# Performance work log

Hardware: AMD Instinct MI355X
Metric: run time of the kernel (lower is better)

Reference implementation:

```python
import jax, jax.numpy as jnp
import numpy as np

N, IN_F, OUT_F = 12288, 256, 128

def setup_inputs() -> dict:
    key = jax.random.key(0)
    k1, k2, k3, k4 = jax.random.split(key, 4)
    x = jax.random.uniform(k1, (N, IN_F), dtype=jnp.float32)
    adj = jax.random.uniform(k2, (N, N), dtype=jnp.float32)
    W = jax.random.normal(k3, (IN_F, OUT_F), dtype=jnp.float32) * (1.0 / np.sqrt(OUT_F))
    b = jax.random.normal(k4, (OUT_F,), dtype=jnp.float32) * (1.0 / np.sqrt(OUT_F))
    return {"x": x, "adj": adj, "W": W, "b": b}

def reference(x, adj, W, b):
    # adj_hat = adj + I  (add self-loops)
    n = adj.shape[0]
    adj_hat = adj + jnp.eye(n, dtype=adj.dtype)
    # Symmetric degree normalization: D^{-1/2} adj_hat D^{-1/2}.
    # Original builds diag matrices and does two NxN matmuls; the math is
    # equivalent to a row/col broadcast scaling, which we use here.
    deg = jnp.sum(adj_hat, axis=1)                  # [N]
    d_inv_sqrt = deg ** -0.5                        # [N]
    adj_norm = adj_hat * d_inv_sqrt[:, None] * d_inv_sqrt[None, :]
    support = x @ W                                 # [N, OUT_F]
    out = adj_norm @ support + b                    # [N, OUT_F]
    return out
```

## Files before the change

### kernel.cpp

```cpp
#include <hip/hip_runtime.h>
#include <cstdint>
#include <cstddef>

#define N_NODES 12288
#define IN_F 256
#define OUT_F 128
#define BM 48
#define BK 256
#define NSTEPS (N_NODES / BK)
#define A_BYTES (BM * BK)
#define B_BYTES (OUT_F * BK)
#define SLOT (A_BYTES + B_BYTES)

using f32x4 = __attribute__((ext_vector_type(4))) float;
typedef long long i64;

__global__ __launch_bounds__(256) void k_deg(const float* __restrict__ adj,
                                             float* __restrict__ dinv,
                                             unsigned int* __restrict__ adjq) {
  const size_t row = blockIdx.x;
  const float4* p = reinterpret_cast<const float4*>(adj + row * N_NODES) + threadIdx.x;
  unsigned int* q = adjq + row * (N_NODES / 4) + threadIdx.x;
  float s = 0.f;
#pragma unroll
  for (int i = 0; i < (N_NODES / 4) / 256; ++i) {
    float4 v = p[(size_t)i * 256];
    s += (v.x + v.y) + (v.z + v.w);
    unsigned int u = (unsigned)__builtin_amdgcn_cvt_pk_fp8_f32(v.x, v.y, 0, false);
    u = (unsigned)__builtin_amdgcn_cvt_pk_fp8_f32(v.z, v.w, (int)u, true);
    q[(size_t)i * 256] = u;
  }
#pragma unroll
  for (int off = 32; off >= 1; off >>= 1) s += __shfl_down(s, off, 64);
  __shared__ float red[4];
  const int lane = threadIdx.x & 63, w = threadIdx.x >> 6;
  if (lane == 0) red[w] = s;
  __syncthreads();
  if (threadIdx.x == 0) {
    float tot = (red[0] + red[1]) + (red[2] + red[3]) + 1.0f;
    dinv[row] = rsqrtf(tot);
  }
}

__global__ __launch_bounds__(256) void k_support(const float* __restrict__ x,
                                                 const float* __restrict__ W,
                                                 const float* __restrict__ dinv,
                                                 float* __restrict__ ssc,
                                                 unsigned char* __restrict__ sTq) {
  const int r = threadIdx.x >> 5;
  const int c4 = (threadIdx.x & 31) << 2;
  const size_t row = (size_t)blockIdx.x * 8 + r;
  const float* xr = x + row * IN_F;
  float a0 = 0.f, a1 = 0.f, a2 = 0.f, a3 = 0.f;
#pragma unroll 4
  for (int k = 0; k < IN_F; ++k) {
    float xv = xr[k];
    float4 wv = *reinterpret_cast<const float4*>(W + (size_t)k * OUT_F + c4);
    a0 = fmaf(xv, wv.x, a0); a1 = fmaf(xv, wv.y, a1);
    a2 = fmaf(xv, wv.z, a2); a3 = fmaf(xv, wv.w, a3);
  }
  const float d = dinv[row];
  a0 *= d; a1 *= d; a2 *= d; a3 *= d;
  *reinterpret_cast<float4*>(ssc + row * OUT_F + c4) = make_float4(a0, a1, a2, a3);
  unsigned int u01 = (unsigned)__builtin_amdgcn_cvt_pk_fp8_f32(a0 * 64.f, a1 * 64.f, 0, false);
  unsigned int u23 = (unsigned)__builtin_amdgcn_cvt_pk_fp8_f32(a2 * 64.f, a3 * 64.f, 0, false);
  sTq[(size_t)(c4 + 0) * N_NODES + row] = (unsigned char)(u01 & 0xff);
  sTq[(size_t)(c4 + 1) * N_NODES + row] = (unsigned char)((u01 >> 8) & 0xff);
  sTq[(size_t)(c4 + 2) * N_NODES + row] = (unsigned char)(u23 & 0xff);
  sTq[(size_t)(c4 + 3) * N_NODES + row] = (unsigned char)((u23 >> 8) & 0xff);
}

__global__ __launch_bounds__(256, 1) void k_gemm(const unsigned char* __restrict__ adjq,
                                                 const unsigned char* __restrict__ sTq,
                                                 const float* __restrict__ ssc,
                                                 const float* __restrict__ dinv,
                                                 const float* __restrict__ bias,
                                                 float* __restrict__ out) {
  __shared__ __align__(16) char LDSBUF[2 * SLOT];

  const int tid = threadIdx.x;
  const int lane = tid & 63;
  const int wv = tid >> 6;
  const size_t rowbase = (size_t)blockIdx.x * BM;

  const int g = lane >> 4;
  const int c15 = lane & 15;
  const int dr = c15 & 7;

  f32x4 acc[3][2];
#pragma unroll
  for (int mt = 0; mt < 3; ++mt)
#pragma unroll
    for (int nt = 0; nt < 2; ++nt) acc[mt][nt] = (f32x4){0.f, 0.f, 0.f, 0.f};

  auto stage = [&](int s, int slot) {
    char* L = LDSBUF + slot * SLOT;
#pragma unroll
    for (int j = 0; j < 3; ++j) {
      const int instr = wv * 3 + j;
      const int r = instr * 4 + g;
      const int chunk = c15 ^ (r & 7);
      const unsigned char* src = adjq + (rowbase + r) * (size_t)N_NODES +
                                 (size_t)s * BK + chunk * 16;
      __builtin_amdgcn_global_load_lds(
          (__attribute__((address_space(1))) void*)src,
          (__attribute__((address_space(3))) void*)(L + instr * 1024 + lane * 16),
          16, 0, 0);
    }
#pragma unroll
    for (int j = 0; j < 8; ++j) {
      const int instr = wv * 8 + j;
      const int o = instr * 4 + g;
      const int chunk = c15 ^ (o & 7);
      const unsigned char* src = sTq + (size_t)o * N_NODES + (size_t)s * BK + chunk * 16;
      __builtin_amdgcn_global_load_lds(
          (__attribute__((address_space(1))) void*)src,
          (__attribute__((address_space(3))) void*)(L + A_BYTES + instr * 1024 + lane * 16),
          16, 0, 0);
    }
  };

  auto compute = [&](int slot) {
    const char* LA = LDSBUF + slot * SLOT;
    const char* LB = LA + A_BYTES;
    const int bcol0 = wv * 32 + c15;
#pragma unroll
    for (int kt = 0; kt < 8; ++kt) {
      const int phys = (((kt * 2 + (g >> 1)) ^ dr) << 4) + ((g & 1) << 3);
      i64 a0 = *(const i64*)(LA + (0 * 16 + c15) * 256 + phys);
      i64 a1 = *(const i64*)(LA + (1 * 16 + c15) * 256 + phys);
      i64 a2 = *(const i64*)(LA + (2 * 16 + c15) * 256 + phys);
      i64 b0 = *(const i64*)(LB + (size_t)(bcol0)*256 + phys);
      i64 b1 = *(const i64*)(LB + (size_t)(bcol0 + 16) * 256 + phys);
      acc[0][0] = __builtin_amdgcn_mfma_f32_16x16x32_fp8_fp8(a0, b0, acc[0][0], 0, 0, 0);
      acc[0][1] = __builtin_amdgcn_mfma_f32_16x16x32_fp8_fp8(a0, b1, acc[0][1], 0, 0, 0);
      acc[1][0] = __builtin_amdgcn_mfma_f32_16x16x32_fp8_fp8(a1, b0, acc[1][0], 0, 0, 0);
      acc[1][1] = __builtin_amdgcn_mfma_f32_16x16x32_fp8_fp8(a1, b1, acc[1][1], 0, 0, 0);
      acc[2][0] = __builtin_amdgcn_mfma_f32_16x16x32_fp8_fp8(a2, b0, acc[2][0], 0, 0, 0);
      acc[2][1] = __builtin_amdgcn_mfma_f32_16x16x32_fp8_fp8(a2, b1, acc[2][1], 0, 0, 0);
    }
  };

#define GSTEP(s, VMC, DOSTAGE)                                   \
  {                                                              \
    asm volatile("s_waitcnt vmcnt(" VMC ")" ::: "memory");       \
    __builtin_amdgcn_s_barrier();                                \
    __builtin_amdgcn_sched_barrier(0);                           \
    compute((s) & 1);                                            \
    __builtin_amdgcn_s_barrier();                                \
    __builtin_amdgcn_sched_barrier(0);                           \
    if (DOSTAGE) stage((s) + 2, (s) & 1);                        \
    __builtin_amdgcn_sched_barrier(0);                           \
  }

  stage(0, 0);
  __builtin_amdgcn_sched_barrier(0);
  stage(1, 1);

  for (int s = 0; s < NSTEPS - 2; ++s) GSTEP(s, "11", 1);
  GSTEP(NSTEPS - 2, "11", 0);
  GSTEP(NSTEPS - 1, "0", 0);
#undef GSTEP

  const float inv64 = 0.015625f;
  const int col0 = wv * 32 + c15;
#pragma unroll
  for (int mt = 0; mt < 3; ++mt) {
#pragma unroll
    for (int nt = 0; nt < 2; ++nt) {
      const int col = col0 + nt * 16;
      const float bv = bias[col];
#pragma unroll
      for (int r = 0; r < 4; ++r) {
        const size_t orow = rowbase + mt * 16 + (g << 2) + r;
        const float d = dinv[orow];
        out[orow * OUT_F + col] =
            fmaf(d, acc[mt][nt][r] * inv64 + ssc[orow * OUT_F + col], bv);
      }
    }
  }
}

extern "C" void kernel_launch(void* const* d_in, const int* in_sizes, int n_in,
                              void* d_out, int out_size, void* d_ws, size_t ws_size,
                              hipStream_t stream) {
  const float* x   = (const float*)d_in[0];
  const float* adj = (const float*)d_in[1];
  const float* W   = (const float*)d_in[2];
  const float* b   = (const float*)d_in[3];
  float* out = (float*)d_out;

  char* ws = (char*)d_ws;
  float* dinv         = (float*)ws;
  float* ssc          = (float*)(ws + 49152);
  unsigned char* sTq  = (unsigned char*)(ws + 49152 + 6291456);
  unsigned char* adjq = (unsigned char*)(ws + 49152 + 6291456 + 1572864);

  k_deg<<<N_NODES, 256, 0, stream>>>(adj, dinv, (unsigned int*)adjq);
  k_support<<<N_NODES / 8, 256, 0, stream>>>(x, W, dinv, ssc, sTq);
  k_gemm<<<256, 256, 0, stream>>>(adjq, sTq, ssc, dinv, b, out);
}
```

Before: 268.3 us.

## Shrink GEMM row tile, load B directly to registers, triple-buffer A with staggered K start

The adjacency GEMM tile drops from 48 to 16 rows, so 768 blocks launch instead of 256, with launch bounds allowing three blocks per CU. The support operand B is now loaded from global memory straight into registers, two steps ahead, instead of through LDS. Only A goes through a three-slot LDS ring. Each block starts its K loop at a different phase, spreading the B reads across cache lines. The degree kernel now uses nontemporal loads for the large fp32 adjacency read. The trade-off is more parallelism and fewer LDS trips against three times as many B reads per output row, plus much higher register pressure from the B buffers.

```diff
diff --git a/kernel.cpp b/kernel.cpp
--- a/kernel.cpp
+++ b/kernel.cpp
@@ -5,12 +5,9 @@
 #define N_NODES 12288
 #define IN_F 256
 #define OUT_F 128
-#define BM 48
+#define BM 16
 #define BK 256
 #define NSTEPS (N_NODES / BK)
-#define A_BYTES (BM * BK)
-#define B_BYTES (OUT_F * BK)
-#define SLOT (A_BYTES + B_BYTES)
 
 using f32x4 = __attribute__((ext_vector_type(4))) float;
 typedef long long i64;
@@ -19,15 +16,15 @@
                                              float* __restrict__ dinv,
                                              unsigned int* __restrict__ adjq) {
   const size_t row = blockIdx.x;
-  const float4* p = reinterpret_cast<const float4*>(adj + row * N_NODES) + threadIdx.x;
+  const f32x4* p = reinterpret_cast<const f32x4*>(adj + row * N_NODES) + threadIdx.x;
   unsigned int* q = adjq + row * (N_NODES / 4) + threadIdx.x;
   float s = 0.f;
 #pragma unroll
   for (int i = 0; i < (N_NODES / 4) / 256; ++i) {
-    float4 v = p[(size_t)i * 256];
-    s += (v.x + v.y) + (v.z + v.w);
-    unsigned int u = (unsigned)__builtin_amdgcn_cvt_pk_fp8_f32(v.x, v.y, 0, false);
-    u = (unsigned)__builtin_amdgcn_cvt_pk_fp8_f32(v.z, v.w, (int)u, true);
+    f32x4 v = __builtin_nontemporal_load(p + (size_t)i * 256);
+    s += (v[0] + v[1]) + (v[2] + v[3]);
+    unsigned int u = (unsigned)__builtin_amdgcn_cvt_pk_fp8_f32(v[0], v[1], 0, false);
+    u = (unsigned)__builtin_amdgcn_cvt_pk_fp8_f32(v[2], v[3], (int)u, true);
     q[(size_t)i * 256] = u;
   }
 #pragma unroll
@@ -70,113 +67,109 @@
   sTq[(size_t)(c4 + 3) * N_NODES + row] = (unsigned char)((u23 >> 8) & 0xff);
 }
 
-__global__ __launch_bounds__(256, 1) void k_gemm(const unsigned char* __restrict__ adjq,
+__global__ __launch_bounds__(256, 3) void k_gemm(const unsigned char* __restrict__ adjq,
                                                  const unsigned char* __restrict__ sTq,
                                                  const float* __restrict__ ssc,
                                                  const float* __restrict__ dinv,
                                                  const float* __restrict__ bias,
                                                  float* __restrict__ out) {
-  __shared__ __align__(16) char LDSBUF[2 * SLOT];
+  __shared__ __align__(16) char A_lds[3 * 4096];
 
   const int tid = threadIdx.x;
   const int lane = tid & 63;
   const int wv = tid >> 6;
   const size_t rowbase = (size_t)blockIdx.x * BM;
+  const int ph = blockIdx.x % NSTEPS;
 
   const int g = lane >> 4;
   const int c15 = lane & 15;
-  const int dr = c15 & 7;
 
-  f32x4 acc[3][2];
+  const int srow = wv * 4 + (lane >> 4);
+  const int schunk = (c15 ^ (srow & 7)) << 4;
+  const unsigned char* abase = adjq + (rowbase + srow) * (size_t)N_NODES + schunk;
+
+  const unsigned char* bptr = sTq + (size_t)(wv * 32 + c15) * N_NODES + g * 8;
+
+  f32x4 acc[2];
+  acc[0] = (f32x4){0.f, 0.f, 0.f, 0.f};
+  acc[1] = (f32x4){0.f, 0.f, 0.f, 0.f};
+
+  i64 b0[2][8], b1[2][8], b2[2][8];
+
+  auto phys = [&](int t) { int c = t + ph; if (c >= NSTEPS) c -= NSTEPS; return c; };
+
+  auto stageA = [&](int t, int slot) {
+    const int sc = phys(t);
+    __builtin_amdgcn_global_load_lds(
+        (__attribute__((address_space(1))) void*)(abase + (size_t)sc * BK),
+        (__attribute__((address_space(3))) void*)(A_lds + slot * 4096 + srow * 256 +
+                                                  (c15 << 4)),
+        16, 0, 0);
+  };
+  auto loadB = [&](int t, i64 (&B)[2][8]) {
+    const int sc = phys(t);
 #pragma unroll
-  for (int mt = 0; mt < 3; ++mt)
+    for (int nt = 0; nt < 2; ++nt)
 #pragma unroll
-    for (int nt = 0; nt < 2; ++nt) acc[mt][nt] = (f32x4){0.f, 0.f, 0.f, 0.f};
-
-  auto stage = [&](int s, int slot) {
-    char* L = LDSBUF + slot * SLOT;
+      for (int kt = 0; kt < 8; ++kt)
+        B[nt][kt] = *(const i64*)(bptr + (size_t)nt * 16 * N_NODES +
+                                  (size_t)sc * BK + kt * 32);
+  };
+  auto compute = [&](int slot, i64 (&B)[2][8]) {
+    const char* Ab = A_lds + slot * 4096 + c15 * 256;
+    const int key = c15 & 7;
 #pragma unroll
-    for (int j = 0; j < 3; ++j) {
-      const int instr = wv * 3 + j;
-      const int r = instr * 4 + g;
-      const int chunk = c15 ^ (r & 7);
-      const unsigned char* src = adjq + (rowbase + r) * (size_t)N_NODES +
-                                 (size_t)s * BK + chunk * 16;
-      __builtin_amdgcn_global_load_lds(
-          (__attribute__((address_space(1))) void*)src,
-          (__attribute__((address_space(3))) void*)(L + instr * 1024 + lane * 16),
-          16, 0, 0);
-    }
-#pragma unroll
-    for (int j = 0; j < 8; ++j) {
-      const int instr = wv * 8 + j;
-      const int o = instr * 4 + g;
-      const int chunk = c15 ^ (o & 7);
-      const unsigned char* src = sTq + (size_t)o * N_NODES + (size_t)s * BK + chunk * 16;
-      __builtin_amdgcn_global_load_lds(
-          (__attribute__((address_space(1))) void*)src,
-          (__attribute__((address_space(3))) void*)(L + A_BYTES + instr * 1024 + lane * 16),
-          16, 0, 0);
+    for (int kt = 0; kt < 8; ++kt) {
+      i64 a = *(const i64*)(Ab + (((kt * 2 + (g >> 1)) ^ key) << 4) + ((g & 1) << 3));
+      acc[0] = __builtin_amdgcn_mfma_f32_16x16x32_fp8_fp8(a, B[0][kt], acc[0], 0, 0, 0);
+      acc[1] = __builtin_amdgcn_mfma_f32_16x16x32_fp8_fp8(a, B[1][kt], acc[1], 0, 0, 0);
     }
   };
 
-  auto compute = [&](int slot) {
-    const char* LA = LDSBUF + slot * SLOT;
-    const char* LB = LA + A_BYTES;
-    const int bcol0 = wv * 32 + c15;
-#pragma unroll
-    for (int kt = 0; kt < 8; ++kt) {
-      const int phys = (((kt * 2 + (g >> 1)) ^ dr) << 4) + ((g & 1) << 3);
-      i64 a0 = *(const i64*)(LA + (0 * 16 + c15) * 256 + phys);
-      i64 a1 = *(const i64*)(LA + (1 * 16 + c15) * 256 + phys);
-      i64 a2 = *(const i64*)(LA + (2 * 16 + c15) * 256 + phys);
-      i64 b0 = *(const i64*)(LB + (size_t)(bcol0)*256 + phys);
-      i64 b1 = *(const i64*)(LB + (size_t)(bcol0 + 16) * 256 + phys);
-      acc[0][0] = __builtin_amdgcn_mfma_f32_16x16x32_fp8_fp8(a0, b0, acc[0][0], 0, 0, 0);
-      acc[0][1] = __builtin_amdgcn_mfma_f32_16x16x32_fp8_fp8(a0, b1, acc[0][1], 0, 0, 0);
-      acc[1][0] = __builtin_amdgcn_mfma_f32_16x16x32_fp8_fp8(a1, b0, acc[1][0], 0, 0, 0);
-      acc[1][1] = __builtin_amdgcn_mfma_f32_16x16x32_fp8_fp8(a1, b1, acc[1][1], 0, 0, 0);
-      acc[2][0] = __builtin_amdgcn_mfma_f32_16x16x32_fp8_fp8(a2, b0, acc[2][0], 0, 0, 0);
-      acc[2][1] = __builtin_amdgcn_mfma_f32_16x16x32_fp8_fp8(a2, b1, acc[2][1], 0, 0, 0);
-    }
-  };
-
-#define GSTEP(s, VMC, DOSTAGE)                                   \
+#define GSTEP(t, S, CUR, NX2, DOPRE, VMC)                        \
   {                                                              \
     asm volatile("s_waitcnt vmcnt(" VMC ")" ::: "memory");       \
     __builtin_amdgcn_s_barrier();                                \
     __builtin_amdgcn_sched_barrier(0);                           \
-    compute((s) & 1);                                            \
-    __builtin_amdgcn_s_barrier();                                \
-    __builtin_amdgcn_sched_barrier(0);                           \
-    if (DOSTAGE) stage((s) + 2, (s) & 1);                        \
-    __builtin_amdgcn_sched_barrier(0);                           \
+    if (DOPRE) {                                                 \
+      loadB((t) + 2, NX2);                                       \
+      __builtin_amdgcn_sched_barrier(0);                         \
+      stageA((t) + 2, ((S) + 2) % 3);                            \
+      __builtin_amdgcn_sched_barrier(0);                         \
+    }                                                            \
+    compute((S), CUR);                                           \
   }
 
-  stage(0, 0);
+  stageA(0, 0);
   __builtin_amdgcn_sched_barrier(0);
-  stage(1, 1);
+  loadB(0, b0);
+  __builtin_amdgcn_sched_barrier(0);
+  stageA(1, 1);
+  __builtin_amdgcn_sched_barrier(0);
+  loadB(1, b1);
+  __builtin_amdgcn_sched_barrier(0);
 
-  for (int s = 0; s < NSTEPS - 2; ++s) GSTEP(s, "11", 1);
-  GSTEP(NSTEPS - 2, "11", 0);
-  GSTEP(NSTEPS - 1, "0", 0);
+  for (int t = 0; t < NSTEPS - 3; t += 3) {
+    GSTEP(t, 0, b0, b2, 1, "17");
+    GSTEP(t + 1, 1, b1, b0, 1, "17");
+    GSTEP(t + 2, 2, b2, b1, 1, "17");
+  }
+  GSTEP(NSTEPS - 3, 0, b0, b2, 1, "17");
+  GSTEP(NSTEPS - 2, 1, b1, b0, 0, "17");
+  GSTEP(NSTEPS - 1, 2, b2, b1, 0, "0");
 #undef GSTEP
 
   const float inv64 = 0.015625f;
-  const int col0 = wv * 32 + c15;
 #pragma unroll
-  for (int mt = 0; mt < 3; ++mt) {
+  for (int nt = 0; nt < 2; ++nt) {
+    const int col = wv * 32 + nt * 16 + c15;
+    const float bv = bias[col];
 #pragma unroll
-    for (int nt = 0; nt < 2; ++nt) {
-      const int col = col0 + nt * 16;
-      const float bv = bias[col];
-#pragma unroll
-      for (int r = 0; r < 4; ++r) {
-        const size_t orow = rowbase + mt * 16 + (g << 2) + r;
-        const float d = dinv[orow];
-        out[orow * OUT_F + col] =
-            fmaf(d, acc[mt][nt][r] * inv64 + ssc[orow * OUT_F + col], bv);
-      }
+    for (int r = 0; r < 4; ++r) {
+      const size_t orow = rowbase + (g << 2) + r;
+      const float d = dinv[orow];
+      out[orow * OUT_F + col] =
+          fmaf(d, acc[nt][r] * inv64 + ssc[orow * OUT_F + col], bv);
     }
   }
 }
@@ -198,5 +191,5 @@
 
   k_deg<<<N_NODES, 256, 0, stream>>>(adj, dinv, (unsigned int*)adjq);
   k_support<<<N_NODES / 8, 256, 0, stream>>>(x, W, dinv, ssc, sTq);
-  k_gemm<<<256, 256, 0, stream>>>(adjq, sTq, ssc, dinv, b, out);
+  k_gemm<<<N_NODES / BM, 256, 0, stream>>>(adjq, sTq, ssc, dinv, b, out);
 }
```

Result: slower. 442.5 us (+64.9%).

## Grid-stride the degree/quantize pass with per-wave partial sums and a separate reduce

Applied to the files above, without the earlier changes.

The row-per-block degree kernel becomes a persistent grid of 2048 blocks. Each wave grid-strides over contiguous 1 KB chunks of adj, converts them to fp8 and writes one partial row sum per chunk. A new small kernel reduces the 48 partials per row and computes the inverse square root of the degree. This aims to improve streaming efficiency and cut the per-block launch and LDS reduction overhead on the 600 MB read, in exchange for an extra launch and a partials buffer.

```diff
diff --git a/kernel.cpp b/kernel.cpp
--- a/kernel.cpp
+++ b/kernel.cpp
@@ -12,34 +12,48 @@
 #define B_BYTES (OUT_F * BK)
 #define SLOT (A_BYTES + B_BYTES)
 
+#define DEG_BLOCKS 2048
+#define DEG_WAVES (DEG_BLOCKS * 4)
+#define N_CHUNKS (N_NODES * N_NODES / 256)
+#define CHUNKS_PER_ROW (N_NODES / 256)
+#define DEG_ITERS (N_CHUNKS / DEG_WAVES)
+
 using f32x4 = __attribute__((ext_vector_type(4))) float;
 typedef long long i64;
 
 __global__ __launch_bounds__(256) void k_deg(const float* __restrict__ adj,
-                                             float* __restrict__ dinv,
-                                             unsigned int* __restrict__ adjq) {
-  const size_t row = blockIdx.x;
-  const float4* p = reinterpret_cast<const float4*>(adj + row * N_NODES) + threadIdx.x;
-  unsigned int* q = adjq + row * (N_NODES / 4) + threadIdx.x;
+                                             unsigned int* __restrict__ adjq,
+                                             float* __restrict__ partials) {
+  const int lane = threadIdx.x & 63;
+  const int wv = threadIdx.x >> 6;
+  const int gw = blockIdx.x * 4 + wv;
+#pragma unroll 4
+  for (int i = 0; i < DEG_ITERS; ++i) {
+    const size_t c = (size_t)gw + (size_t)i * DEG_WAVES;
+    const size_t f4 = c * 64 + lane;
+    f32x4 v = *(reinterpret_cast<const f32x4*>(adj) + f4);
+    unsigned int u = (unsigned)__builtin_amdgcn_cvt_pk_fp8_f32(v[0], v[1], 0, false);
+    u = (unsigned)__builtin_amdgcn_cvt_pk_fp8_f32(v[2], v[3], (int)u, true);
+    adjq[f4] = u;
+    float s = (v[0] + v[1]) + (v[2] + v[3]);
+    s += __shfl_xor(s, 1, 64);
+    s += __shfl_xor(s, 2, 64);
+    s += __shfl_xor(s, 4, 64);
+    s += __shfl_xor(s, 8, 64);
+    s += __shfl_xor(s, 16, 64);
+    s += __shfl_xor(s, 32, 64);
+    if (lane == 0) partials[c] = s;
+  }
+}
+
+__global__ __launch_bounds__(256) void k_dinv(const float* __restrict__ partials,
+                                              float* __restrict__ dinv) {
+  const int r = blockIdx.x * 256 + threadIdx.x;
+  const float* p = partials + (size_t)r * CHUNKS_PER_ROW;
   float s = 0.f;
 #pragma unroll
-  for (int i = 0; i < (N_NODES / 4) / 256; ++i) {
-    float4 v = p[(size_t)i * 256];
-    s += (v.x + v.y) + (v.z + v.w);
-    unsigned int u = (unsigned)__builtin_amdgcn_cvt_pk_fp8_f32(v.x, v.y, 0, false);
-    u = (unsigned)__builtin_amdgcn_cvt_pk_fp8_f32(v.z, v.w, (int)u, true);
-    q[(size_t)i * 256] = u;
-  }
-#pragma unroll
-  for (int off = 32; off >= 1; off >>= 1) s += __shfl_down(s, off, 64);
-  __shared__ float red[4];
-  const int lane = threadIdx.x & 63, w = threadIdx.x >> 6;
-  if (lane == 0) red[w] = s;
-  __syncthreads();
-  if (threadIdx.x == 0) {
-    float tot = (red[0] + red[1]) + (red[2] + red[3]) + 1.0f;
-    dinv[row] = rsqrtf(tot);
-  }
+  for (int k = 0; k < CHUNKS_PER_ROW; ++k) s += p[k];
+  dinv[r] = rsqrtf(1.f + s);
 }
 
 __global__ __launch_bounds__(256) void k_support(const float* __restrict__ x,
@@ -195,8 +209,10 @@
   float* ssc          = (float*)(ws + 49152);
   unsigned char* sTq  = (unsigned char*)(ws + 49152 + 6291456);
   unsigned char* adjq = (unsigned char*)(ws + 49152 + 6291456 + 1572864);
-
-  k_deg<<<N_NODES, 256, 0, stream>>>(adj, dinv, (unsigned int*)adjq);
+  float* partials     = (float*)(ws + 49152 + 6291456 + 1572864 + 150994944);
+
+  k_deg<<<DEG_BLOCKS, 256, 0, stream>>>(adj, (unsigned int*)adjq, partials);
+  k_dinv<<<N_NODES / 256, 256, 0, stream>>>(partials, dinv);
   k_support<<<N_NODES / 8, 256, 0, stream>>>(x, W, dinv, ssc, sTq);
-  k_gemm<<<256, 256, 0, stream>>>(adjq, sTq, ssc, dinv, b, out);
-}
+  k_gemm<<<N_NODES / BM, 256, 0, stream>>>(adjq, sTq, ssc, dinv, b, out);
+}
```

Result: slower. 275.2 us (+2.6%).
